# Performance work log

Hardware: AMD Instinct MI355X
Metric: run time of the kernel (lower is better)

Reference implementation:

```python
import jax, jax.numpy as jnp
import numpy as np

D_PAIR = 128
D_HIDDEN = 128
EPS = 1e-5


def layer_norm(x, w, b):
    mu = jnp.mean(x, axis=-1, keepdims=True)
    var = jnp.var(x, axis=-1, keepdims=True)
    return (x - mu) * jax.lax.rsqrt(var + EPS) * w + b


def setup_inputs() -> dict:
    key = jax.random.key(0)
    ks = jax.random.split(key, 8)
    B, N, D, H = 1, 512, D_PAIR, D_HIDDEN
    pair = jax.random.normal(ks[0], (B, N, N, D), dtype=jnp.float32)
    # torch Linear weight layout: [out_features, in_features]
    p_in_w = jax.random.normal(ks[1], (2 * H, D), dtype=jnp.float32) / np.sqrt(D)
    g_in_w = jax.random.normal(ks[2], (2 * H, D), dtype=jnp.float32) / np.sqrt(D)
    p_out_w = jax.random.normal(ks[3], (D, H), dtype=jnp.float32) / np.sqrt(H)
    g_out_w = jax.random.normal(ks[4], (D, D), dtype=jnp.float32) / np.sqrt(D)
    ln_in_w = jnp.ones((D,), jnp.float32)
    ln_in_b = jnp.zeros((D,), jnp.float32)
    ln_out_w = jnp.ones((H,), jnp.float32)
    ln_out_b = jnp.zeros((H,), jnp.float32)
    return {
        "pair": pair,
        "ln_in_w": ln_in_w, "ln_in_b": ln_in_b,
        "p_in_w": p_in_w, "g_in_w": g_in_w,
        "ln_out_w": ln_out_w, "ln_out_b": ln_out_b,
        "p_out_w": p_out_w, "g_out_w": g_out_w,
    }


def reference(pair, ln_in_w, ln_in_b, p_in_w, g_in_w, ln_out_w, ln_out_b, p_out_w, g_out_w):
    H = D_HIDDEN
    L = pair.shape[1]
    pair_norm = layer_norm(pair, ln_in_w, ln_in_b)           # [B,N,N,D]
    p = jnp.einsum('bijd,hd->bijh', pair_norm, p_in_w)       # [B,N,N,2H]
    g = jax.nn.sigmoid(jnp.einsum('bijd,hd->bijh', pair_norm, g_in_w))
    left = g[..., :H] * p[..., :H]
    right = g[..., H:] * p[..., H:]
    # outgoing direction
    out = jnp.einsum('bikd,bjkd->bijd', left, right / jnp.float32(L))
    out = layer_norm(out, ln_out_w, ln_out_b)
    out = jnp.einsum('bijh,dh->bijd', out, p_out_w)
    gate = jax.nn.sigmoid(jnp.einsum('bijd,ed->bije', pair_norm, g_out_w))
    return gate * out
```

## Files before the change

kernel.cpp:

```cpp
#include <hip/hip_runtime.h>

#define NSEQ 512
#define RTOT (NSEQ*NSEQ)
#define DM 128

typedef unsigned short ushort_t;
using short8 = __attribute__((ext_vector_type(8))) short;
using f32x4  = __attribute__((ext_vector_type(4))) float;

__device__ __forceinline__ unsigned short f2bf(float x){
  union { float f; unsigned int u; } v; v.f = x;
  unsigned int r = v.u + 0x7fffu + ((v.u >> 16) & 1u);
  return (unsigned short)(r >> 16);
}
__device__ __forceinline__ float bf2f(unsigned short u){
  union { unsigned int u; float f; } v; v.u = ((unsigned int)u) << 16;
  return v.f;
}
__device__ __forceinline__ unsigned int pack2(float a, float b){
  return (unsigned int)f2bf(a) | ((unsigned int)f2bf(b) << 16);
}
__device__ __forceinline__ float sigmoidf(float x){ return 1.0f/(1.0f + __expf(-x)); }

__global__ __launch_bounds__(256) void k_prep(const float* __restrict__ a,
                                              const float* __restrict__ b,
                                              ushort_t* __restrict__ da,
                                              ushort_t* __restrict__ db,
                                              int na4, int nb4){
  int idx = blockIdx.x*256 + threadIdx.x;
  const float* src; ushort_t* dst; int i;
  if (idx < na4){ src = a; dst = da; i = idx; }
  else { i = idx - na4; if (i >= nb4) return; src = b; dst = db; }
  float4 v = *(const float4*)(src + (size_t)i*4);
  uint2 pk; pk.x = pack2(v.x, v.y); pk.y = pack2(v.z, v.w);
  *(uint2*)(dst + (size_t)i*4) = pk;
}

__global__ __launch_bounds__(256) void k0_ln_in(const float* __restrict__ pair,
                                                const float* __restrict__ w,
                                                const float* __restrict__ b,
                                                ushort_t* __restrict__ lnx){
  int wv = threadIdx.x >> 6, lane = threadIdx.x & 63;
  size_t row = (size_t)blockIdx.x * 4 + wv;
  const float2* src = (const float2*)(pair + row * DM);
  float2 v = src[lane];
  float s = v.x + v.y, s2 = v.x*v.x + v.y*v.y;
  #pragma unroll
  for (int off = 32; off; off >>= 1){ s += __shfl_xor(s, off); s2 += __shfl_xor(s2, off); }
  float mu = s * (1.f/DM);
  float rstd = rsqrtf(s2*(1.f/DM) - mu*mu + 1e-5f);
  float o0 = (v.x - mu)*rstd*w[2*lane]   + b[2*lane];
  float o1 = (v.y - mu)*rstd*w[2*lane+1] + b[2*lane+1];
  ((unsigned int*)(lnx + row * DM))[lane] = pack2(o0, o1);
}

__global__ __launch_bounds__(256) void k1_inproj(const ushort_t* __restrict__ lnx,
                                                 const ushort_t* __restrict__ pw_bf,
                                                 const ushort_t* __restrict__ gw_bf,
                                                 ushort_t* __restrict__ left,
                                                 ushort_t* __restrict__ right){
  __shared__ __align__(16) ushort_t A[64][136];
  __shared__ __align__(16) ushort_t B[128][136];
  int tid = threadIdx.x;
  int job = blockIdx.x;
  int bm  = blockIdx.y;
  int wrow0 = ((job >= 2) ? 128 : 0) + (job & 1) * 64;
  ushort_t* outp = (job >= 2) ? right : left;
  int dbase = (job & 1) * 64;
  size_t arow0 = (size_t)bm * 64;

  #pragma unroll
  for (int it = 0; it < 4; it++){
    int e = (tid + it*256) * 8; int r = e >> 7, c = e & 127;
    *(uint4*)&A[r][c] = *(const uint4*)&lnx[(arow0 + r)*DM + c];
  }
  #pragma unroll
  for (int it = 0; it < 8; it++){
    int e = (tid + it*256) * 8; int r = e >> 7, c = e & 127;
    const ushort_t* srcw = (r < 64) ? &pw_bf[(size_t)(wrow0 + r)*DM + c]
                                    : &gw_bf[(size_t)(wrow0 + r - 64)*DM + c];
    *(uint4*)&B[r][c] = *(const uint4*)srcw;
  }
  __syncthreads();

  int w = tid >> 6, lane = tid & 63, m = lane & 15, quad = lane >> 4;
  f32x4 acc[8];
  #pragma unroll
  for (int i = 0; i < 8; i++) acc[i] = (f32x4){0.f,0.f,0.f,0.f};
  #pragma unroll
  for (int k0 = 0; k0 < 128; k0 += 32){
    short8 a = *(const short8*)&A[w*16 + m][k0 + quad*8];
    #pragma unroll
    for (int c = 0; c < 8; c++){
      short8 bf = *(const short8*)&B[c*16 + m][k0 + quad*8];
      acc[c] = __builtin_amdgcn_mfma_f32_16x16x32_bf16(a, bf, acc[c], 0, 0, 0);
    }
  }
  size_t r0 = arow0 + w*16 + quad*4;
  #pragma unroll
  for (int c = 0; c < 4; c++){
    int d = dbase + c*16 + m;
    uint2 pk;
    pk.x = pack2(sigmoidf(acc[c+4][0]) * acc[c][0], sigmoidf(acc[c+4][1]) * acc[c][1]);
    pk.y = pack2(sigmoidf(acc[c+4][2]) * acc[c][2], sigmoidf(acc[c+4][3]) * acc[c][3]);
    *(uint2*)&outp[(size_t)d * RTOT + r0] = pk;
  }
}

__global__ __launch_bounds__(256) void k2_tri(const ushort_t* __restrict__ left,
                                              const ushort_t* __restrict__ right,
                                              ushort_t* __restrict__ tri){
  __shared__ __align__(16) ushort_t As[128][72];
  __shared__ __align__(16) ushort_t Bs[128][72];
  int tid = threadIdx.x;
  int b = blockIdx.x;
  int d = b & 127, ti = b >> 7;
  const ushort_t* Ap = left  + (size_t)d * RTOT;
  const ushort_t* Bp = right + (size_t)d * RTOT;
  ushort_t* Cp = tri + (size_t)d * RTOT;
  int i0 = ti * 128;
  int w = tid >> 6, lane = tid & 63, m = lane & 15, quad = lane >> 4;
  int wr = w & 1, wc = w >> 1;

  for (int tj = 0; tj < 4; tj++){
    int j0 = tj * 128;
    f32x4 acc[16];
    #pragma unroll
    for (int x = 0; x < 16; x++) acc[x] = (f32x4){0.f,0.f,0.f,0.f};

    for (int kt = 0; kt < NSEQ; kt += 64){
      __syncthreads();
      #pragma unroll
      for (int it = 0; it < 4; it++){
        int e = (tid + it*256) * 8; int r = e >> 6, c = e & 63;
        *(uint4*)&As[r][c] = *(const uint4*)&Ap[(size_t)(i0 + r)*NSEQ + kt + c];
        *(uint4*)&Bs[r][c] = *(const uint4*)&Bp[(size_t)(j0 + r)*NSEQ + kt + c];
      }
      __syncthreads();
      #pragma unroll
      for (int kk = 0; kk < 64; kk += 32){
        short8 a[4], bb[4];
        #pragma unroll
        for (int t = 0; t < 4; t++) a[t]  = *(const short8*)&As[wr*64 + t*16 + m][kk + quad*8];
        #pragma unroll
        for (int c = 0; c < 4; c++) bb[c] = *(const short8*)&Bs[wc*64 + c*16 + m][kk + quad*8];
        #pragma unroll
        for (int t = 0; t < 4; t++){
          #pragma unroll
          for (int c = 0; c < 4; c++){
            acc[t*4+c] = __builtin_amdgcn_mfma_f32_16x16x32_bf16(a[t], bb[c], acc[t*4+c], 0, 0, 0);
          }
        }
      }
    }
    const float s = 1.f / (float)NSEQ;
    #pragma unroll
    for (int t = 0; t < 4; t++){
      #pragma unroll
      for (int c = 0; c < 4; c++){
        int col = j0 + wc*64 + c*16 + m;
        #pragma unroll
        for (int rr = 0; rr < 4; rr++){
          int row = i0 + wr*64 + t*16 + quad*4 + rr;
          Cp[(size_t)row * NSEQ + col] = f2bf(acc[t*4+c][rr] * s);
        }
      }
    }
  }
}

__global__ __launch_bounds__(256) void k3_out(const ushort_t* __restrict__ tri,
                                              const ushort_t* __restrict__ lnx,
                                              const float* __restrict__ lnw,
                                              const float* __restrict__ lnb,
                                              const ushort_t* __restrict__ pow_bf,
                                              const ushort_t* __restrict__ gow_bf,
                                              float* __restrict__ out){
  __shared__ __align__(16) ushort_t A1[64][136];
  __shared__ __align__(16) ushort_t A2[64][136];
  __shared__ __align__(16) ushort_t Bt[64][136];
  __shared__ float lw[128], lb[128];
  int tid = threadIdx.x;
  size_t r0 = (size_t)blockIdx.x * 64;

  if (tid < 128){ lw[tid] = lnw[tid]; lb[tid] = lnb[tid]; }
  #pragma unroll
  for (int it = 0; it < 4; it++){
    int e = (tid + it*256) * 8; int r = e >> 7, c = e & 127;
    *(uint4*)&A2[r][c] = *(const uint4*)&lnx[(r0 + r)*DM + c];
  }
  {
    int dch = tid >> 1, half = tid & 1;
    const ushort_t* src = tri + (size_t)dch * RTOT + r0 + half*32;
    #pragma unroll
    for (int q = 0; q < 4; q++){
      uint4 v = *(const uint4*)(src + q*8);
      int rb = half*32 + q*8;
      A1[rb+0][dch] = (ushort_t)(v.x & 0xffff); A1[rb+1][dch] = (ushort_t)(v.x >> 16);
      A1[rb+2][dch] = (ushort_t)(v.y & 0xffff); A1[rb+3][dch] = (ushort_t)(v.y >> 16);
      A1[rb+4][dch] = (ushort_t)(v.z & 0xffff); A1[rb+5][dch] = (ushort_t)(v.z >> 16);
      A1[rb+6][dch] = (ushort_t)(v.w & 0xffff); A1[rb+7][dch] = (ushort_t)(v.w >> 16);
    }
  }
  __syncthreads();
  {
    int row = tid >> 2, part = tid & 3;
    float x[32]; float s = 0.f, s2 = 0.f;
    #pragma unroll
    for (int j = 0; j < 32; j++){ x[j] = bf2f(A1[row][part*32 + j]); s += x[j]; s2 += x[j]*x[j]; }
    s += __shfl_xor(s, 1); s2 += __shfl_xor(s2, 1);
    s += __shfl_xor(s, 2); s2 += __shfl_xor(s2, 2);
    float mu = s * (1.f/DM);
    float rstd = rsqrtf(s2*(1.f/DM) - mu*mu + 1e-5f);
    #pragma unroll
    for (int j = 0; j < 32; j++){
      int cc = part*32 + j;
      A1[row][cc] = f2bf((x[j] - mu)*rstd*lw[cc] + lb[cc]);
    }
  }
  __syncthreads();

  int w = tid >> 6, lane = tid & 63, m = lane & 15, quad = lane >> 4;
  #pragma unroll
  for (int ch = 0; ch < 2; ch++){
    f32x4 accp[4], accg[4];
    #pragma unroll
    for (int i = 0; i < 4; i++){ accp[i] = (f32x4){0.f,0.f,0.f,0.f}; accg[i] = (f32x4){0.f,0.f,0.f,0.f}; }

    #pragma unroll
    for (int it = 0; it < 4; it++){
      int e = (tid + it*256) * 8; int r = e >> 7, c = e & 127;
      *(uint4*)&Bt[r][c] = *(const uint4*)&pow_bf[(size_t)(ch*64 + r)*DM + c];
    }
    __syncthreads();
    #pragma unroll
    for (int k0 = 0; k0 < 128; k0 += 32){
      short8 a = *(const short8*)&A1[w*16 + m][k0 + quad*8];
      #pragma unroll
      for (int c = 0; c < 4; c++){
        short8 bf = *(const short8*)&Bt[c*16 + m][k0 + quad*8];
        accp[c] = __builtin_amdgcn_mfma_f32_16x16x32_bf16(a, bf, accp[c], 0, 0, 0);
      }
    }
    __syncthreads();
    #pragma unroll
    for (int it = 0; it < 4; it++){
      int e = (tid + it*256) * 8; int r = e >> 7, c = e & 127;
      *(uint4*)&Bt[r][c] = *(const uint4*)&gow_bf[(size_t)(ch*64 + r)*DM + c];
    }
    __syncthreads();
    #pragma unroll
    for (int k0 = 0; k0 < 128; k0 += 32){
      short8 a = *(const short8*)&A2[w*16 + m][k0 + quad*8];
      #pragma unroll
      for (int c = 0; c < 4; c++){
        short8 bf = *(const short8*)&Bt[c*16 + m][k0 + quad*8];
        accg[c] = __builtin_amdgcn_mfma_f32_16x16x32_bf16(a, bf, accg[c], 0, 0, 0);
      }
    }
    #pragma unroll
    for (int c = 0; c < 4; c++){
      int dcol = ch*64 + c*16 + m;
      #pragma unroll
      for (int rr = 0; rr < 4; rr++){
        size_t row = r0 + w*16 + quad*4 + rr;
        out[row * DM + dcol] = sigmoidf(accg[c][rr]) * accp[c][rr];
      }
    }
    __syncthreads();
  }
}

extern "C" void kernel_launch(void* const* d_in, const int* in_sizes, int n_in,
                              void* d_out, int out_size, void* d_ws, size_t ws_size,
                              hipStream_t stream){
  const float* pair     = (const float*)d_in[0];
  const float* ln_in_w  = (const float*)d_in[1];
  const float* ln_in_b  = (const float*)d_in[2];
  const float* p_in_w   = (const float*)d_in[3];
  const float* g_in_w   = (const float*)d_in[4];
  const float* ln_out_w = (const float*)d_in[5];
  const float* ln_out_b = (const float*)d_in[6];
  const float* p_out_w  = (const float*)d_in[7];
  const float* g_out_w  = (const float*)d_in[8];
  float* out = (float*)d_out;

  const size_t plane = (size_t)RTOT * DM;
  ushort_t* lnx   = (ushort_t*)d_ws;
  ushort_t* left  = lnx   + plane;
  ushort_t* right = left  + plane;
  ushort_t* tri   = right + plane;

  ushort_t* pw_bf  = tri;
  ushort_t* gw_bf  = tri + 32768;
  ushort_t* pow_bf = left;
  ushort_t* gow_bf = left + 16384;

  k_prep   <<<dim3(64),          dim3(256), 0, stream>>>(p_in_w, g_in_w, pw_bf, gw_bf, 8192, 8192);
  k0_ln_in <<<dim3(RTOT/4),      dim3(256), 0, stream>>>(pair, ln_in_w, ln_in_b, lnx);
  k1_inproj<<<dim3(4, RTOT/64),  dim3(256), 0, stream>>>(lnx, pw_bf, gw_bf, left, right);
  k2_tri   <<<dim3(512),         dim3(256), 0, stream>>>(left, right, tri);
  k_prep   <<<dim3(32),          dim3(256), 0, stream>>>(p_out_w, g_out_w, pow_bf, gow_bf, 4096, 4096);
  k3_out   <<<dim3(RTOT/64),     dim3(256), 0, stream>>>(tri, lnx, ln_out_w, ln_out_b,
                                                         pow_bf, gow_bf, out);
}
```

Baseline: 462.4 us.

## Fold output layernorm into projection weights and restructure in-proj with register-held weights

The output layernorm is folded algebraically into the output projection. A single-block prep kernel premultiplies p_out_w by ln_out_w and precomputes per-column correction sums, so k3 only computes per-row mean and rstd and applies them in the epilogue. The tri transpose load is rewritten to gather 8 channels per short8 while accumulating statistics, and the lnx operand is read straight from global into registers. k1 keeps its weight fragments in registers, processes 256 rows per block, and drops shared-memory staging. The trade-off is more uncoalesced global reads of lnx in k1 and strided 2-byte gathers from tri in k3.

```diff
diff --git a/kernel.cpp b/kernel.cpp
--- a/kernel.cpp
+++ b/kernel.cpp
@@ -36,6 +36,34 @@
   *(uint2*)(dst + (size_t)i*4) = pk;
 }
 
+__global__ __launch_bounds__(256) void k_prep2(const float* __restrict__ p_out_w,
+                                               const float* __restrict__ g_out_w,
+                                               const float* __restrict__ ln_out_w,
+                                               const float* __restrict__ ln_out_b,
+                                               ushort_t* __restrict__ wp,
+                                               ushort_t* __restrict__ wg,
+                                               float2* __restrict__ c12){
+  int t = threadIdx.x;
+  if (t < 128){
+    float s1 = 0.f, s2 = 0.f;
+    for (int d = 0; d < DM; d++){
+      float v = p_out_w[(size_t)t*DM + d];
+      unsigned short h = f2bf(v * ln_out_w[d]);
+      wp[(size_t)t*DM + d] = h;
+      s1 += bf2f(h);
+      s2 += ln_out_b[d] * v;
+    }
+    c12[t] = make_float2(s1, s2);
+  } else {
+    int r = t - 128;
+    for (int d = 0; d < DM; d += 4){
+      float4 v = *(const float4*)&g_out_w[(size_t)r*DM + d];
+      uint2 pk; pk.x = pack2(v.x, v.y); pk.y = pack2(v.z, v.w);
+      *(uint2*)&wg[(size_t)r*DM + d] = pk;
+    }
+  }
+}
+
 __global__ __launch_bounds__(256) void k0_ln_in(const float* __restrict__ pair,
                                                 const float* __restrict__ w,
                                                 const float* __restrict__ b,
@@ -59,51 +87,45 @@
                                                  const ushort_t* __restrict__ gw_bf,
                                                  ushort_t* __restrict__ left,
                                                  ushort_t* __restrict__ right){
-  __shared__ __align__(16) ushort_t A[64][136];
-  __shared__ __align__(16) ushort_t B[128][136];
   int tid = threadIdx.x;
+  int wc = tid >> 6, lane = tid & 63, m = lane & 15, quad = lane >> 4;
   int job = blockIdx.x;
-  int bm  = blockIdx.y;
   int wrow0 = ((job >= 2) ? 128 : 0) + (job & 1) * 64;
   ushort_t* outp = (job >= 2) ? right : left;
-  int dbase = (job & 1) * 64;
-  size_t arow0 = (size_t)bm * 64;
-
-  #pragma unroll
-  for (int it = 0; it < 4; it++){
-    int e = (tid + it*256) * 8; int r = e >> 7, c = e & 127;
-    *(uint4*)&A[r][c] = *(const uint4*)&lnx[(arow0 + r)*DM + c];
-  }
-  #pragma unroll
-  for (int it = 0; it < 8; it++){
-    int e = (tid + it*256) * 8; int r = e >> 7, c = e & 127;
-    const ushort_t* srcw = (r < 64) ? &pw_bf[(size_t)(wrow0 + r)*DM + c]
-                                    : &gw_bf[(size_t)(wrow0 + r - 64)*DM + c];
-    *(uint4*)&B[r][c] = *(const uint4*)srcw;
-  }
-  __syncthreads();
-
-  int w = tid >> 6, lane = tid & 63, m = lane & 15, quad = lane >> 4;
-  f32x4 acc[8];
-  #pragma unroll
-  for (int i = 0; i < 8; i++) acc[i] = (f32x4){0.f,0.f,0.f,0.f};
-  #pragma unroll
-  for (int k0 = 0; k0 < 128; k0 += 32){
-    short8 a = *(const short8*)&A[w*16 + m][k0 + quad*8];
-    #pragma unroll
-    for (int c = 0; c < 8; c++){
-      short8 bf = *(const short8*)&B[c*16 + m][k0 + quad*8];
-      acc[c] = __builtin_amdgcn_mfma_f32_16x16x32_bf16(a, bf, acc[c], 0, 0, 0);
-    }
-  }
-  size_t r0 = arow0 + w*16 + quad*4;
-  #pragma unroll
-  for (int c = 0; c < 4; c++){
-    int d = dbase + c*16 + m;
-    uint2 pk;
-    pk.x = pack2(sigmoidf(acc[c+4][0]) * acc[c][0], sigmoidf(acc[c+4][1]) * acc[c][1]);
-    pk.y = pack2(sigmoidf(acc[c+4][2]) * acc[c][2], sigmoidf(acc[c+4][3]) * acc[c][3]);
-    *(uint2*)&outp[(size_t)d * RTOT + r0] = pk;
+  int d = (job & 1) * 64 + wc*16 + m;
+  size_t row0 = (size_t)blockIdx.y * 256;
+
+  const ushort_t* prow = pw_bf + (size_t)(wrow0 + wc*16 + m)*DM + quad*8;
+  const ushort_t* grow = gw_bf + (size_t)(wrow0 + wc*16 + m)*DM + quad*8;
+  short8 bp[4], bg[4];
+  #pragma unroll
+  for (int k = 0; k < 4; k++){
+    bp[k] = *(const short8*)(prow + k*32);
+    bg[k] = *(const short8*)(grow + k*32);
+  }
+
+  #pragma unroll
+  for (int ch = 0; ch < 4; ch++){
+    size_t r0 = row0 + ch*64;
+    f32x4 accp[4], accg[4];
+    #pragma unroll
+    for (int i = 0; i < 4; i++){ accp[i] = (f32x4){0.f,0.f,0.f,0.f}; accg[i] = (f32x4){0.f,0.f,0.f,0.f}; }
+    #pragma unroll
+    for (int k = 0; k < 4; k++){
+      #pragma unroll
+      for (int rt = 0; rt < 4; rt++){
+        short8 a = *(const short8*)&lnx[(r0 + rt*16 + m)*DM + k*32 + quad*8];
+        accp[rt] = __builtin_amdgcn_mfma_f32_16x16x32_bf16(a, bp[k], accp[rt], 0, 0, 0);
+        accg[rt] = __builtin_amdgcn_mfma_f32_16x16x32_bf16(a, bg[k], accg[rt], 0, 0, 0);
+      }
+    }
+    #pragma unroll
+    for (int rt = 0; rt < 4; rt++){
+      uint2 pk;
+      pk.x = pack2(sigmoidf(accg[rt][0])*accp[rt][0], sigmoidf(accg[rt][1])*accp[rt][1]);
+      pk.y = pack2(sigmoidf(accg[rt][2])*accp[rt][2], sigmoidf(accg[rt][3])*accp[rt][3]);
+      *(uint2*)&outp[(size_t)d * RTOT + r0 + rt*16 + quad*4] = pk;
+    }
   }
 }
 
@@ -171,56 +193,58 @@
 
 __global__ __launch_bounds__(256) void k3_out(const ushort_t* __restrict__ tri,
                                               const ushort_t* __restrict__ lnx,
-                                              const float* __restrict__ lnw,
-                                              const float* __restrict__ lnb,
-                                              const ushort_t* __restrict__ pow_bf,
-                                              const ushort_t* __restrict__ gow_bf,
+                                              const ushort_t* __restrict__ wp,
+                                              const ushort_t* __restrict__ wg,
+                                              const float2* __restrict__ c12,
                                               float* __restrict__ out){
   __shared__ __align__(16) ushort_t A1[64][136];
-  __shared__ __align__(16) ushort_t A2[64][136];
   __shared__ __align__(16) ushort_t Bt[64][136];
-  __shared__ float lw[128], lb[128];
+  __shared__ float ss[64][4], sq[64][4];
+  __shared__ float2 srow[64];
+  __shared__ float2 c12s[128];
   int tid = threadIdx.x;
   size_t r0 = (size_t)blockIdx.x * 64;
-
-  if (tid < 128){ lw[tid] = lnw[tid]; lb[tid] = lnb[tid]; }
-  #pragma unroll
-  for (int it = 0; it < 4; it++){
-    int e = (tid + it*256) * 8; int r = e >> 7, c = e & 127;
-    *(uint4*)&A2[r][c] = *(const uint4*)&lnx[(r0 + r)*DM + c];
-  }
+  if (tid < 128) c12s[tid] = c12[tid];
+
+  int j = tid & 63, wv = tid >> 6;
   {
-    int dch = tid >> 1, half = tid & 1;
-    const ushort_t* src = tri + (size_t)dch * RTOT + r0 + half*32;
-    #pragma unroll
-    for (int q = 0; q < 4; q++){
-      uint4 v = *(const uint4*)(src + q*8);
-      int rb = half*32 + q*8;
-      A1[rb+0][dch] = (ushort_t)(v.x & 0xffff); A1[rb+1][dch] = (ushort_t)(v.x >> 16);
-      A1[rb+2][dch] = (ushort_t)(v.y & 0xffff); A1[rb+3][dch] = (ushort_t)(v.y >> 16);
-      A1[rb+4][dch] = (ushort_t)(v.z & 0xffff); A1[rb+5][dch] = (ushort_t)(v.z >> 16);
-      A1[rb+6][dch] = (ushort_t)(v.w & 0xffff); A1[rb+7][dch] = (ushort_t)(v.w >> 16);
-    }
+    float fs = 0.f, fq = 0.f;
+    #pragma unroll
+    for (int g = 0; g < 4; g++){
+      int oct = wv*4 + g;
+      const ushort_t* src = tri + (size_t)(oct*8)*RTOT + r0 + j;
+      short8 v;
+      #pragma unroll
+      for (int dd = 0; dd < 8; dd++){
+        unsigned short u = src[(size_t)dd * RTOT];
+        v[dd] = (short)u;
+        float f = bf2f(u); fs += f; fq += f*f;
+      }
+      *(short8*)&A1[j][oct*8] = v;
+    }
+    ss[j][wv] = fs; sq[j][wv] = fq;
   }
   __syncthreads();
-  {
-    int row = tid >> 2, part = tid & 3;
-    float x[32]; float s = 0.f, s2 = 0.f;
-    #pragma unroll
-    for (int j = 0; j < 32; j++){ x[j] = bf2f(A1[row][part*32 + j]); s += x[j]; s2 += x[j]*x[j]; }
-    s += __shfl_xor(s, 1); s2 += __shfl_xor(s2, 1);
-    s += __shfl_xor(s, 2); s2 += __shfl_xor(s2, 2);
+  if (tid < 64){
+    float s = ss[tid][0]+ss[tid][1]+ss[tid][2]+ss[tid][3];
+    float q = sq[tid][0]+sq[tid][1]+sq[tid][2]+sq[tid][3];
     float mu = s * (1.f/DM);
-    float rstd = rsqrtf(s2*(1.f/DM) - mu*mu + 1e-5f);
-    #pragma unroll
-    for (int j = 0; j < 32; j++){
-      int cc = part*32 + j;
-      A1[row][cc] = f2bf((x[j] - mu)*rstd*lw[cc] + lb[cc]);
-    }
+    float rstd = rsqrtf(q*(1.f/DM) - mu*mu + 1e-5f);
+    srow[tid] = make_float2(mu, rstd);
   }
   __syncthreads();
 
-  int w = tid >> 6, lane = tid & 63, m = lane & 15, quad = lane >> 4;
+  int lane = tid & 63, m = lane & 15, quad = lane >> 4;
+  short8 a1[4], a2[4];
+  #pragma unroll
+  for (int k = 0; k < 4; k++){
+    a1[k] = *(const short8*)&A1[wv*16 + m][k*32 + quad*8];
+    a2[k] = *(const short8*)&lnx[(r0 + wv*16 + m)*DM + k*32 + quad*8];
+  }
+  float2 st[4];
+  #pragma unroll
+  for (int rr = 0; rr < 4; rr++) st[rr] = srow[wv*16 + quad*4 + rr];
+
   #pragma unroll
   for (int ch = 0; ch < 2; ch++){
     f32x4 accp[4], accg[4];
@@ -230,41 +254,40 @@
     #pragma unroll
     for (int it = 0; it < 4; it++){
       int e = (tid + it*256) * 8; int r = e >> 7, c = e & 127;
-      *(uint4*)&Bt[r][c] = *(const uint4*)&pow_bf[(size_t)(ch*64 + r)*DM + c];
+      *(uint4*)&Bt[r][c] = *(const uint4*)&wp[(size_t)(ch*64 + r)*DM + c];
     }
     __syncthreads();
     #pragma unroll
-    for (int k0 = 0; k0 < 128; k0 += 32){
-      short8 a = *(const short8*)&A1[w*16 + m][k0 + quad*8];
+    for (int k = 0; k < 4; k++){
       #pragma unroll
       for (int c = 0; c < 4; c++){
-        short8 bf = *(const short8*)&Bt[c*16 + m][k0 + quad*8];
-        accp[c] = __builtin_amdgcn_mfma_f32_16x16x32_bf16(a, bf, accp[c], 0, 0, 0);
+        short8 bf = *(const short8*)&Bt[c*16 + m][k*32 + quad*8];
+        accp[c] = __builtin_amdgcn_mfma_f32_16x16x32_bf16(a1[k], bf, accp[c], 0, 0, 0);
       }
     }
     __syncthreads();
     #pragma unroll
     for (int it = 0; it < 4; it++){
       int e = (tid + it*256) * 8; int r = e >> 7, c = e & 127;
-      *(uint4*)&Bt[r][c] = *(const uint4*)&gow_bf[(size_t)(ch*64 + r)*DM + c];
+      *(uint4*)&Bt[r][c] = *(const uint4*)&wg[(size_t)(ch*64 + r)*DM + c];
     }
     __syncthreads();
     #pragma unroll
-    for (int k0 = 0; k0 < 128; k0 += 32){
-      short8 a = *(const short8*)&A2[w*16 + m][k0 + quad*8];
+    for (int k = 0; k < 4; k++){
       #pragma unroll
       for (int c = 0; c < 4; c++){
-        short8 bf = *(const short8*)&Bt[c*16 + m][k0 + quad*8];
-        accg[c] = __builtin_amdgcn_mfma_f32_16x16x32_bf16(a, bf, accg[c], 0, 0, 0);
+        short8 bf = *(const short8*)&Bt[c*16 + m][k*32 + quad*8];
+        accg[c] = __builtin_amdgcn_mfma_f32_16x16x32_bf16(a2[k], bf, accg[c], 0, 0, 0);
       }
     }
     #pragma unroll
     for (int c = 0; c < 4; c++){
-      int dcol = ch*64 + c*16 + m;
+      int h = ch*64 + c*16 + m;
+      float2 cc = c12s[h];
       #pragma unroll
       for (int rr = 0; rr < 4; rr++){
-        size_t row = r0 + w*16 + quad*4 + rr;
-        out[row * DM + dcol] = sigmoidf(accg[c][rr]) * accp[c][rr];
+        float val = st[rr].y * (accp[c][rr] - st[rr].x * cc.x) + cc.y;
+        out[(r0 + wv*16 + quad*4 + rr)*DM + h] = sigmoidf(accg[c][rr]) * val;
       }
     }
     __syncthreads();
@@ -291,16 +314,16 @@
   ushort_t* right = left  + plane;
   ushort_t* tri   = right + plane;
 
-  ushort_t* pw_bf  = tri;
-  ushort_t* gw_bf  = tri + 32768;
-  ushort_t* pow_bf = left;
-  ushort_t* gow_bf = left + 16384;
+  ushort_t* pw_bf = tri;
+  ushort_t* gw_bf = tri + 32768;
+  ushort_t* wp    = left;
+  ushort_t* wg    = left + 16384;
+  float2*   c12   = (float2*)(left + 32768);
 
   k_prep   <<<dim3(64),          dim3(256), 0, stream>>>(p_in_w, g_in_w, pw_bf, gw_bf, 8192, 8192);
   k0_ln_in <<<dim3(RTOT/4),      dim3(256), 0, stream>>>(pair, ln_in_w, ln_in_b, lnx);
-  k1_inproj<<<dim3(4, RTOT/64),  dim3(256), 0, stream>>>(lnx, pw_bf, gw_bf, left, right);
+  k1_inproj<<<dim3(4, RTOT/256), dim3(256), 0, stream>>>(lnx, pw_bf, gw_bf, left, right);
   k2_tri   <<<dim3(512),         dim3(256), 0, stream>>>(left, right, tri);
-  k_prep   <<<dim3(32),          dim3(256), 0, stream>>>(p_out_w, g_out_w, pow_bf, gow_bf, 4096, 4096);
-  k3_out   <<<dim3(RTOT/64),     dim3(256), 0, stream>>>(tri, lnx, ln_out_w, ln_out_b,
-                                                         pow_bf, gow_bf, out);
-}
+  k_prep2  <<<dim3(1),           dim3(256), 0, stream>>>(p_out_w, g_out_w, ln_out_w, ln_out_b, wp, wg, c12);
+  k3_out   <<<dim3(RTOT/64),     dim3(256), 0, stream>>>(tri, lnx, wp, wg, c12, out);
+}
```

Result: slower. 525.2 us (+13.6%).
